# Kernel tuning notes

Measured on AMD Instinct MI355X. Metric: run time of the kernel, lower is better.

Reference implementation:

```python
import jax, jax.numpy as jnp
import numpy as np

BN_EPS = 1e-5
ALPHA = 0.3
NEG = -9e9
BN_SCALE = 1.0 / np.sqrt(1.0 + BN_EPS)  # eval BatchNorm with running_mean=0, running_var=1


def gat_layer(x, mask, W, a, bn_g, bn_b, concat):
    # x: [B,N,Fin], mask: [B,N,N] bool, W: [Fin,Fo], a: [2*Fo]
    h = jnp.einsum('bnf,fo->bno', x, W)               # [B,N,Fo]
    Fo = W.shape[1]
    s1 = h @ a[:Fo]                                    # [B,N]
    s2 = h @ a[Fo:]                                    # [B,N]
    # additive decomposition of concat([h_i, h_j]) @ a (identical math)
    e = jax.nn.leaky_relu(s1[:, :, None] + s2[:, None, :], ALPHA)  # [B,N,N]
    att = jax.nn.softmax(jnp.where(mask, e, NEG), axis=-1)
    hp = jnp.einsum('bnm,bmo->bno', att, h)            # [B,N,Fo]
    # BatchNorm1d(nodes_num) in eval mode, per-node-channel affine
    hp = hp * BN_SCALE * bn_g[None, :, None] + bn_b[None, :, None]
    return jax.nn.elu(hp) if concat else hp


def setup_inputs() -> dict:
    key = jax.random.key(0)
    ks = jax.random.split(key, 10)
    B, N, F, Fo, H, C = 128, 200, 768, 32, 8, 2
    Fh = Fo * H
    return {
        'feat_matrix': jax.random.normal(ks[0], (B, N, F), jnp.float32),
        'adj': jax.random.randint(ks[1], (B, N, N), 0, 2, jnp.int32),
        'W_heads': jax.random.normal(ks[2], (H, F, Fo), jnp.float32) * 0.05,
        'a_heads': jax.random.normal(ks[3], (H, 2 * Fo), jnp.float32) * 0.1,
        'bnh_g': jnp.ones((H, N), jnp.float32),
        'bnh_b': jnp.zeros((H, N), jnp.float32),
        'bnt_g': jnp.ones((N,), jnp.float32),
        'bnt_b': jnp.zeros((N,), jnp.float32),
        'W_sent': jax.random.normal(ks[4], (Fh, C), jnp.float32) * 0.1,
        'a_sent': jax.random.normal(ks[5], (2 * C,), jnp.float32) * 0.1,
        'bns_g': jnp.ones((N,), jnp.float32),
        'bns_b': jnp.zeros((N,), jnp.float32),
        'W_para': jax.random.normal(ks[6], (Fh, C), jnp.float32) * 0.1,
        'a_para': jax.random.normal(ks[7], (2 * C,), jnp.float32) * 0.1,
        'bnp_g': jnp.ones((N,), jnp.float32),
        'bnp_b': jnp.zeros((N,), jnp.float32),
        'W_q': jax.random.normal(ks[8], (Fh, Fo), jnp.float32) * 0.1,
        'a_q': jax.random.normal(ks[9], (2 * Fo,), jnp.float32) * 0.1,
        'bnq_g': jnp.ones((N,), jnp.float32),
        'bnq_b': jnp.zeros((N,), jnp.float32),
        'W2': jax.random.normal(jax.random.fold_in(key, 99), (Fo, 2), jnp.float32) * 0.1,
    }


def reference(feat_matrix, adj, W_heads, a_heads, bnh_g, bnh_b, bnt_g, bnt_b,
              W_sent, a_sent, bns_g, bns_b, W_para, a_para, bnp_g, bnp_b,
              W_q, a_q, bnq_g, bnq_b, W2):
    mask = adj > 0
    # 8 attention heads (concat=True), vmapped over head dim
    heads = jax.vmap(lambda W, a, g, b: gat_layer(feat_matrix, mask, W, a, g, b, True))(
        W_heads, a_heads, bnh_g, bnh_b)              # [H,B,N,Fo]
    H, B, N, Fo = heads.shape
    x = jnp.moveaxis(heads, 0, 2).reshape(B, N, H * Fo)  # head-major concat, matches torch.cat
    # top-level BatchNorm1d (eval) + dropout(no-op)
    x = x * BN_SCALE * bnt_g[None, :, None] + bnt_b[None, :, None]
    logits_sent = jax.nn.sigmoid(gat_layer(x, mask, W_sent, a_sent, bns_g, bns_b, False))
    logits_para = jax.nn.elu(gat_layer(x, mask, W_para, a_para, bnp_g, bnp_b, False))
    q = gat_layer(x, mask, W_q, a_q, bnq_g, bnq_b, False)[:, 0, :]   # [B,Fo]
    logits_Qtype = jax.nn.elu(q @ W2).reshape(-1, 2)
    return (logits_sent, logits_para, logits_Qtype)
```

## Files before the change

kernel.cpp:

```cpp
#include <hip/hip_runtime.h>
#include <hip/hip_bf16.h>
#include <cstdint>

#define BN_SCALEF 0.99999500003749975f
#define EXP_SHIFT 4.0f


typedef _Float16 half8 __attribute__((ext_vector_type(8)));
typedef _Float16 half4 __attribute__((ext_vector_type(4)));
typedef float floatx4 __attribute__((ext_vector_type(4)));


__global__ void pack_mask(const int* __restrict__ adj, unsigned int* __restrict__ maskw) {
    int bi = blockIdx.x;
    int t  = threadIdx.x;
    bool v = false;
    if (t < 200) v = adj[(size_t)bi * 200 + t] > 0;
    unsigned long long m = __ballot(v ? 1 : 0);
    if ((t & 63) == 0) {
        maskw[bi * 8 + (t >> 6) * 2 + 0] = (unsigned int)(m & 0xffffffffULL);
        maskw[bi * 8 + (t >> 6) * 2 + 1] = (unsigned int)(m >> 32);
    }
}

__global__ void build_wcat_t(const float* __restrict__ W_heads, _Float16* __restrict__ Bt) {
    int c = blockIdx.x;
    int h = c >> 5, o = c & 31;
    for (int f = threadIdx.x; f < 768; f += 256)
        Bt[(size_t)c * 768 + f] = (_Float16)W_heads[h * (768 * 32) + f * 32 + o];
}

__global__ void build_w2t(const float* __restrict__ Ws, const float* __restrict__ Wp,
                          const float* __restrict__ Wq, float* __restrict__ W2t) {
    int c = blockIdx.x;
    int k = threadIdx.x;
    float v;
    if (c < 2)      v = Ws[k * 2 + c];
    else if (c < 4) v = Wp[k * 2 + (c - 2)];
    else            v = Wq[k * 32 + (c - 4)];
    W2t[c * 256 + k] = v;
}


__global__ __launch_bounds__(512) void gemm1_mfma(const float* __restrict__ A,
                                                  const _Float16* __restrict__ Bt,
                                                  const float* __restrict__ a_h,
                                                  float* __restrict__ C,
                                                  float* __restrict__ s1,
                                                  float* __restrict__ s2) {
    __shared__ __align__(16) _Float16 As[128 * 40];
    __shared__ __align__(16) _Float16 Bs[256 * 40];
    int t = threadIdx.x;
    int m0 = blockIdx.x * 128;
    int w = t >> 6, lane = t & 63;
    int wr = w >> 2, wc = w & 3;
    int quad = lane >> 4, l16 = lane & 15;

    floatx4 acc[4][4];
#pragma unroll
    for (int i = 0; i < 4; ++i)
#pragma unroll
        for (int j = 0; j < 4; ++j) acc[i][j] = (floatx4){0.f, 0.f, 0.f, 0.f};

    int arow = t >> 2, akoff = (t & 3) * 8;
    int bcol = t >> 1, bkoff = (t & 1) * 16;
    const float*    Aptr = &A[(size_t)(m0 + arow) * 768 + akoff];
    const _Float16* Bptr = &Bt[(size_t)bcol * 768 + bkoff];

    float4 pa0 = *(const float4*)(Aptr);
    float4 pa1 = *(const float4*)(Aptr + 4);
    uint4  pb0 = *(const uint4*)(Bptr);
    uint4  pb1 = *(const uint4*)(Bptr + 8);

    for (int k0 = 0; k0 < 768; k0 += 32) {
        half8 ah;
        ah[0] = (_Float16)pa0.x; ah[1] = (_Float16)pa0.y;
        ah[2] = (_Float16)pa0.z; ah[3] = (_Float16)pa0.w;
        ah[4] = (_Float16)pa1.x; ah[5] = (_Float16)pa1.y;
        ah[6] = (_Float16)pa1.z; ah[7] = (_Float16)pa1.w;
        *(half8*)&As[arow * 40 + akoff] = ah;
        *(uint4*)&Bs[bcol * 40 + bkoff]     = pb0;
        *(uint4*)&Bs[bcol * 40 + bkoff + 8] = pb1;
        __syncthreads();
        if (k0 + 32 < 768) {
            pa0 = *(const float4*)(Aptr + k0 + 32);
            pa1 = *(const float4*)(Aptr + k0 + 36);
            pb0 = *(const uint4*)(Bptr + k0 + 32);
            pb1 = *(const uint4*)(Bptr + k0 + 40);
        }
        half8 af[4], bf[4];
#pragma unroll
        for (int rt = 0; rt < 4; ++rt)
            af[rt] = *(half8*)&As[(wr * 64 + rt * 16 + l16) * 40 + quad * 8];
#pragma unroll
        for (int ct = 0; ct < 4; ++ct)
            bf[ct] = *(half8*)&Bs[(wc * 64 + ct * 16 + l16) * 40 + quad * 8];
#pragma unroll
        for (int rt = 0; rt < 4; ++rt)
#pragma unroll
            for (int ct = 0; ct < 4; ++ct)
                acc[rt][ct] = __builtin_amdgcn_mfma_f32_16x16x32_f16(af[rt], bf[ct], acc[rt][ct], 0, 0, 0);
        __syncthreads();
    }

    int rbase = m0 + wr * 64;
    int cbase = wc * 64;
#pragma unroll
    for (int rt = 0; rt < 4; ++rt)
#pragma unroll
        for (int ct = 0; ct < 4; ++ct) {
            int gc = cbase + ct * 16 + l16;
#pragma unroll
            for (int r = 0; r < 4; ++r) {
                int gr = rbase + rt * 16 + quad * 4 + r;
                C[(size_t)gr * 256 + gc] = acc[rt][ct][r];
            }
        }
#pragma unroll
    for (int hh = 0; hh < 2; ++hh) {
        int h0 = wc * 2 + hh;
        const float* ab = &a_h[h0 * 64];
        float a1l = ab[l16], a1h = ab[16 + l16];
        float a2l = ab[32 + l16], a2h = ab[48 + l16];
#pragma unroll
        for (int rt = 0; rt < 4; ++rt)
#pragma unroll
            for (int r = 0; r < 4; ++r) {
                float v0 = acc[rt][2 * hh][r], v1 = acc[rt][2 * hh + 1][r];
                float p1 = v0 * a1l + v1 * a1h;
                float p2 = v0 * a2l + v1 * a2h;
                p1 += __shfl_xor(p1, 1, 64); p1 += __shfl_xor(p1, 2, 64);
                p1 += __shfl_xor(p1, 4, 64); p1 += __shfl_xor(p1, 8, 64);
                p2 += __shfl_xor(p2, 1, 64); p2 += __shfl_xor(p2, 2, 64);
                p2 += __shfl_xor(p2, 4, 64); p2 += __shfl_xor(p2, 8, 64);
                if (l16 == 0) {
                    int gr = rbase + rt * 16 + quad * 4 + r;
                    s1[h0 * 25600 + gr] = p1;
                    s2[h0 * 25600 + gr] = p2;
                }
            }
    }
}


__global__ __launch_bounds__(256) void attn_heads_mfma(
    const float* __restrict__ h_all, const float* __restrict__ s1g, const float* __restrict__ s2g,
    const unsigned int* __restrict__ maskw,
    const float* __restrict__ bnh_g, const float* __restrict__ bnh_b,
    const float* __restrict__ bnt_g, const float* __restrict__ bnt_b,
    float* __restrict__ x_cat) {
    __shared__ __align__(16) _Float16 Bs[48 * 232];
    __shared__ __align__(16) _Float16 Ps[64 * 232];
    int hb = blockIdx.x;
    int h = hb >> 7, b = hb & 127;
    int t = threadIdx.x;

    unsigned long long* bz = (unsigned long long*)Bs;
    for (int idx = t; idx < (48 * 232) / 4; idx += 256) bz[idx] = 0ULL;
    __syncthreads();
    for (int idx = t; idx < 1600; idx += 256) {
        int j = idx >> 3, w4 = (idx & 7) * 4;
        float4 v = *(const float4*)&h_all[(size_t)(b * 200 + j) * 256 + h * 32 + w4];
        Bs[(w4 + 0) * 232 + j] = (_Float16)v.x;
        Bs[(w4 + 1) * 232 + j] = (_Float16)v.y;
        Bs[(w4 + 2) * 232 + j] = (_Float16)v.z;
        Bs[(w4 + 3) * 232 + j] = (_Float16)v.w;
    }
    if (t < 200) Bs[32 * 232 + t] = (_Float16)1.0f;
    __syncthreads();

    int w = t >> 6, lane = t & 63;
    int l16 = lane & 15, quad = lane >> 4;
    _Float16* Pw = &Ps[w * 16 * 232];

    int j0 = lane * 4;
    float4 s2r = {0.f, 0.f, 0.f, 0.f};
    if (j0 + 3 < 200) {
        s2r = *(const float4*)&s2g[(size_t)(h * 128 + b) * 200 + j0];
    } else if (j0 < 200) {
        const float* sp = &s2g[(size_t)(h * 128 + b) * 200];
        float tmp[4] = {0.f, 0.f, 0.f, 0.f};
        for (int q = 0; q < 4 && j0 + q < 200; ++q) tmp[q] = sp[j0 + q];
        s2r = {tmp[0], tmp[1], tmp[2], tmp[3]};
    }
    const float* s1p = &s1g[(size_t)(h * 128 + b) * 200];

    for (int tile = w; tile < 13; tile += 4) {
        int i_base = tile * 16;
        int nrows = (i_base + 16 <= 200) ? 16 : (200 - i_base);
        for (int r16 = 0; r16 < nrows; ++r16) {
            int i = i_base + r16;
            float s1v = s1p[i];
            unsigned int mw = maskw[(size_t)(b * 200 + i) * 8 + (lane >> 3)];
            half4 pv;
#pragma unroll
            for (int q = 0; q < 4; ++q) {
                float e = s1v + ((const float*)&s2r)[q];
                e = fmaxf(e, 0.3f * e);
                float p = ((mw >> ((j0 + q) & 31)) & 1u) ? __expf(e - EXP_SHIFT) : 0.f;
                pv[q] = (_Float16)p;
            }
            if (j0 < 224) *(half4*)&Pw[r16 * 232 + j0] = pv;
        }
        floatx4 acc0 = {0.f, 0.f, 0.f, 0.f};
        floatx4 acc1 = {0.f, 0.f, 0.f, 0.f};
        floatx4 acc2 = {0.f, 0.f, 0.f, 0.f};
#pragma unroll
        for (int kt = 0; kt < 7; ++kt) {
            half8 af = *(half8*)&Pw[l16 * 232 + kt * 32 + quad * 8];
            half8 b0 = *(half8*)&Bs[(l16) * 232 + kt * 32 + quad * 8];
            half8 b1 = *(half8*)&Bs[(16 + l16) * 232 + kt * 32 + quad * 8];
            half8 b2 = *(half8*)&Bs[(32 + l16) * 232 + kt * 32 + quad * 8];
            acc0 = __builtin_amdgcn_mfma_f32_16x16x32_f16(af, b0, acc0, 0, 0, 0);
            acc1 = __builtin_amdgcn_mfma_f32_16x16x32_f16(af, b1, acc1, 0, 0, 0);
            acc2 = __builtin_amdgcn_mfma_f32_16x16x32_f16(af, b2, acc2, 0, 0, 0);
        }
#pragma unroll
        for (int r = 0; r < 4; ++r) {
            int i = i_base + quad * 4 + r;
            float rsum = __shfl(acc2[r], (lane & 48), 64);
            if (i < 200) {
                float inv = 1.f / rsum;
                float g1 = BN_SCALEF * bnh_g[h * 200 + i], c1 = bnh_b[h * 200 + i];
                float g2 = BN_SCALEF * bnt_g[i], c2 = bnt_b[i];
                float v0 = acc0[r] * inv * g1 + c1;
                v0 = v0 > 0.f ? v0 : __expf(v0) - 1.f;
                v0 = v0 * g2 + c2;
                float v1 = acc1[r] * inv * g1 + c1;
                v1 = v1 > 0.f ? v1 : __expf(v1) - 1.f;
                v1 = v1 * g2 + c2;
                size_t base = (size_t)(b * 200 + i) * 256 + h * 32;
                x_cat[base + l16]      = v0;
                x_cat[base + 16 + l16] = v1;
            }
        }
    }
}


__global__ __launch_bounds__(256) void gemm2(const float* __restrict__ X,
                                             const float* __restrict__ W2t,
                                             float* __restrict__ H2) {
    __shared__ __align__(16) float Ws[36 * 260];
    int t = threadIdx.x;
#pragma unroll
    for (int rep = 0; rep < 9; ++rep) {
        int fidx = rep * 1024 + t * 4;
        int c = fidx >> 8, k = fidx & 255;
        *(float4*)&Ws[c * 260 + k] = *(const float4*)&W2t[fidx];
    }
    __syncthreads();
    int cg = t & 3, rt = t >> 2;
    int row0 = blockIdx.x * 128 + rt * 2;
    float acc[2][9] = {};
#pragma unroll 2
    for (int k = 0; k < 256; k += 4) {
        float4 x0 = *(const float4*)&X[(size_t)row0 * 256 + k];
        float4 x1 = *(const float4*)&X[(size_t)(row0 + 1) * 256 + k];
#pragma unroll
        for (int c = 0; c < 9; ++c) {
            float4 wv = *(float4*)&Ws[(cg * 9 + c) * 260 + k];
            acc[0][c] += x0.x * wv.x + x0.y * wv.y + x0.z * wv.z + x0.w * wv.w;
            acc[1][c] += x1.x * wv.x + x1.y * wv.y + x1.z * wv.z + x1.w * wv.w;
        }
    }
#pragma unroll
    for (int rr = 0; rr < 2; ++rr)
#pragma unroll
        for (int c = 0; c < 9; ++c)
            H2[(size_t)(row0 + rr) * 36 + cg * 9 + c] = acc[rr][c];
}


__global__ __launch_bounds__(256) void s12_second(const float* __restrict__ H2,
                                                  const float* __restrict__ a_sent,
                                                  const float* __restrict__ a_para,
                                                  const float* __restrict__ a_q,
                                                  float* __restrict__ sv) {
    int row = blockIdx.x * 256 + threadIdx.x;
    const float* hp = &H2[(size_t)row * 36];
    float h0 = hp[0], h1 = hp[1], h2v = hp[2], h3 = hp[3];
    sv[row]          = h0 * a_sent[0] + h1 * a_sent[1];
    sv[25600 + row]  = h0 * a_sent[2] + h1 * a_sent[3];
    sv[51200 + row]  = h2v * a_para[0] + h3 * a_para[1];
    sv[76800 + row]  = h2v * a_para[2] + h3 * a_para[3];
    float aq1 = 0.f, aq2 = 0.f;
#pragma unroll
    for (int o = 0; o < 32; ++o) {
        float hv = hp[4 + o];
        aq1 += hv * a_q[o];
        aq2 += hv * a_q[32 + o];
    }
    sv[102400 + row] = aq1;
    sv[128000 + row] = aq2;
}


__global__ __launch_bounds__(256) void attn_sp(const float* __restrict__ H2,
                                               const float* __restrict__ sv,
                                               const unsigned int* __restrict__ maskw,
                                               const float* __restrict__ bns_g, const float* __restrict__ bns_b,
                                               const float* __restrict__ bnp_g, const float* __restrict__ bnp_b,
                                               float* __restrict__ out) {
    __shared__ float s2s[200], s2p[200];
    __shared__ __align__(16) float hsp[200 * 4];
    int b = blockIdx.x, chunk = blockIdx.y;
    int t = threadIdx.x;
    if (t < 200) {
        s2s[t] = sv[25600 + b * 200 + t];
        s2p[t] = sv[76800 + b * 200 + t];
    }
    for (int idx = t; idx < 800; idx += 256) {
        int j = idx >> 2, c = idx & 3;
        hsp[idx] = H2[(size_t)(b * 200 + j) * 36 + c];
    }
    __syncthreads();
    int w = t >> 6, lane = t & 63;
    for (int it = 0; it < 25; ++it) {
        int i = chunk * 100 + it * 4 + w;
        float s1sv = sv[b * 200 + i];
        float s1pv = sv[51200 + b * 200 + i];
        float ds = 0.f, dp = 0.f, pa0 = 0.f, pa1 = 0.f, pb0 = 0.f, pb1 = 0.f;
#pragma unroll
        for (int q = 0; q < 4; ++q) {
            int j = lane + 64 * q;
            if (j < 200) {
                unsigned int mw = maskw[(size_t)(b * 200 + i) * 8 + (j >> 5)];
                if ((mw >> (j & 31)) & 1u) {
                    float x1 = s1sv + s2s[j]; x1 = fmaxf(x1, 0.3f * x1);
                    float x2 = s1pv + s2p[j]; x2 = fmaxf(x2, 0.3f * x2);
                    float p1 = __expf(x1 - EXP_SHIFT), p2 = __expf(x2 - EXP_SHIFT);
                    ds += p1; dp += p2;
                    float4 hv = *(float4*)&hsp[j * 4];
                    pa0 += p1 * hv.x; pa1 += p1 * hv.y;
                    pb0 += p2 * hv.z; pb1 += p2 * hv.w;
                }
            }
        }
        for (int off = 32; off; off >>= 1) {
            ds  += __shfl_xor(ds, off, 64);  dp  += __shfl_xor(dp, off, 64);
            pa0 += __shfl_xor(pa0, off, 64); pa1 += __shfl_xor(pa1, off, 64);
            pb0 += __shfl_xor(pb0, off, 64); pb1 += __shfl_xor(pb1, off, 64);
        }
        if (lane == 0) {
            float gs = BN_SCALEF * bns_g[i], bs = bns_b[i];
            float v0 = (pa0 / ds) * gs + bs, v1 = (pa1 / ds) * gs + bs;
            out[(size_t)(b * 200 + i) * 2 + 0] = 1.f / (1.f + __expf(-v0));
            out[(size_t)(b * 200 + i) * 2 + 1] = 1.f / (1.f + __expf(-v1));
            float gp = BN_SCALEF * bnp_g[i], bp = bnp_b[i];
            float u0 = (pb0 / dp) * gp + bp, u1 = (pb1 / dp) * gp + bp;
            out[51200 + (size_t)(b * 200 + i) * 2 + 0] = u0 > 0.f ? u0 : __expf(u0) - 1.f;
            out[51200 + (size_t)(b * 200 + i) * 2 + 1] = u1 > 0.f ? u1 : __expf(u1) - 1.f;
        }
    }
}


__global__ __launch_bounds__(256) void attn_q(const float* __restrict__ H2,
                                              const float* __restrict__ sv,
                                              const unsigned int* __restrict__ maskw,
                                              const float* __restrict__ bnq_g, const float* __restrict__ bnq_b,
                                              const float* __restrict__ W2, float* __restrict__ out) {
    __shared__ float p_lds[200];
    __shared__ float redd[4];
    __shared__ float red2[256];
    int b = blockIdx.x, t = threadIdx.x;
    float s1v = sv[102400 + b * 200];
    float p = 0.f;
    if (t < 200) {
        unsigned int mw = maskw[(size_t)(b * 200) * 8 + (t >> 5)];
        if ((mw >> (t & 31)) & 1u) {
            float x = s1v + sv[128000 + b * 200 + t];
            x = fmaxf(x, 0.3f * x);
            p = __expf(x - EXP_SHIFT);
        }
        p_lds[t] = p;
    }
    float ds = p;
    for (int off = 32; off; off >>= 1) ds += __shfl_xor(ds, off, 64);
    if ((t & 63) == 0) redd[t >> 6] = ds;
    __syncthreads();
    ds = redd[0] + redd[1] + redd[2] + redd[3];
    int o = t & 31, g = t >> 5;
    float acc = 0.f;
    for (int j = g; j < 200; j += 8)
        acc += p_lds[j] * H2[(size_t)(b * 200 + j) * 36 + 4 + o];
    red2[t] = acc;
    __syncthreads();
    if (t < 32) {
        float s = 0.f;
#pragma unroll
        for (int gg = 0; gg < 8; ++gg) s += red2[gg * 32 + t];
        float qv = (s / ds) * (BN_SCALEF * bnq_g[0]) + bnq_b[0];
        float c0 = qv * W2[t * 2], c1 = qv * W2[t * 2 + 1];
#pragma unroll
        for (int off = 16; off; off >>= 1) {
            c0 += __shfl_xor(c0, off, 64);
            c1 += __shfl_xor(c1, off, 64);
        }
        if (t == 0) {
            out[102400 + b * 2 + 0] = c0 > 0.f ? c0 : __expf(c0) - 1.f;
            out[102400 + b * 2 + 1] = c1 > 0.f ? c1 : __expf(c1) - 1.f;
        }
    }
}


extern "C" void kernel_launch(void* const* d_in, const int* in_sizes, int n_in,
                              void* d_out, int out_size, void* d_ws, size_t ws_size,
                              hipStream_t stream) {
    (void)in_sizes; (void)n_in; (void)out_size; (void)ws_size;
    const float* feat    = (const float*)d_in[0];
    const int*   adj     = (const int*)d_in[1];
    const float* W_heads = (const float*)d_in[2];
    const float* a_heads = (const float*)d_in[3];
    const float* bnh_g   = (const float*)d_in[4];
    const float* bnh_b   = (const float*)d_in[5];
    const float* bnt_g   = (const float*)d_in[6];
    const float* bnt_b   = (const float*)d_in[7];
    const float* W_sent  = (const float*)d_in[8];
    const float* a_sent  = (const float*)d_in[9];
    const float* bns_g   = (const float*)d_in[10];
    const float* bns_b   = (const float*)d_in[11];
    const float* W_para  = (const float*)d_in[12];
    const float* a_para  = (const float*)d_in[13];
    const float* bnp_g   = (const float*)d_in[14];
    const float* bnp_b   = (const float*)d_in[15];
    const float* W_q     = (const float*)d_in[16];
    const float* a_q     = (const float*)d_in[17];
    const float* bnq_g   = (const float*)d_in[18];
    const float* bnq_b   = (const float*)d_in[19];
    const float* W2      = (const float*)d_in[20];
    float* out = (float*)d_out;
    float* ws  = (float*)d_ws;

    float* h_all = ws;
    float* x_cat = ws + 6553600;
    float* s1h   = ws + 13107200;
    float* s2h   = ws + 13312000;
    float* w2t   = ws + 13516800;
    _Float16* Bt = (_Float16*)(ws + 13526016);
    unsigned int* maskw = (unsigned int*)(ws + 13624320);
    float* h2    = ws + 13829120;
    float* sv    = ws + 14750720;

    pack_mask<<<dim3(25600), dim3(256), 0, stream>>>(adj, maskw);
    build_wcat_t<<<dim3(256), dim3(256), 0, stream>>>(W_heads, Bt);
    build_w2t<<<dim3(36), dim3(256), 0, stream>>>(W_sent, W_para, W_q, w2t);
    gemm1_mfma<<<dim3(200), dim3(512), 0, stream>>>(feat, Bt, a_heads, h_all, s1h, s2h);
    attn_heads_mfma<<<dim3(1024), dim3(256), 0, stream>>>(h_all, s1h, s2h, maskw,
                                                          bnh_g, bnh_b, bnt_g, bnt_b, x_cat);
    gemm2<<<dim3(200), dim3(256), 0, stream>>>(x_cat, w2t, h2);
    s12_second<<<dim3(100), dim3(256), 0, stream>>>(h2, a_sent, a_para, a_q, sv);
    attn_sp<<<dim3(128, 2), dim3(256), 0, stream>>>(h2, sv, maskw, bns_g, bns_b,
                                                    bnp_g, bnp_b, out);
    attn_q<<<dim3(128), dim3(256), 0, stream>>>(h2, sv, maskw, bnq_g, bnq_b, W2, out);
}
```

Before: 318.0 us.

## Merge prep kernels, store intermediates in fp16, shrink gemm1 tile, fuse tail kernels

Three preprocessing kernels become one prep kernel, and the W_heads transpose now goes through shared memory. gemm1 uses 64-row tiles, launching 400 blocks instead of 200 to fill more compute units. h and x_cat are stored as fp16 to halve the intermediate traffic. s12_second is fused into gemm2 and attn_q into attn_sp, cutting the launch count from 9 to 5. The risk is extra fp16 rounding in x_cat ahead of the second-layer GEMM.

Measured after the change: 299.9 us. 5.7% less time.

```diff
diff --git a/kernel.cpp b/kernel.cpp
--- a/kernel.cpp
+++ b/kernel.cpp
@@ -11,109 +11,123 @@
 typedef float floatx4 __attribute__((ext_vector_type(4)));
 
 
-__global__ void pack_mask(const int* __restrict__ adj, unsigned int* __restrict__ maskw) {
-    int bi = blockIdx.x;
-    int t  = threadIdx.x;
-    bool v = false;
-    if (t < 200) v = adj[(size_t)bi * 200 + t] > 0;
-    unsigned long long m = __ballot(v ? 1 : 0);
-    if ((t & 63) == 0) {
-        maskw[bi * 8 + (t >> 6) * 2 + 0] = (unsigned int)(m & 0xffffffffULL);
-        maskw[bi * 8 + (t >> 6) * 2 + 1] = (unsigned int)(m >> 32);
-    }
-}
-
-__global__ void build_wcat_t(const float* __restrict__ W_heads, _Float16* __restrict__ Bt) {
-    int c = blockIdx.x;
-    int h = c >> 5, o = c & 31;
-    for (int f = threadIdx.x; f < 768; f += 256)
-        Bt[(size_t)c * 768 + f] = (_Float16)W_heads[h * (768 * 32) + f * 32 + o];
-}
-
-__global__ void build_w2t(const float* __restrict__ Ws, const float* __restrict__ Wp,
-                          const float* __restrict__ Wq, float* __restrict__ W2t) {
-    int c = blockIdx.x;
-    int k = threadIdx.x;
-    float v;
-    if (c < 2)      v = Ws[k * 2 + c];
-    else if (c < 4) v = Wp[k * 2 + (c - 2)];
-    else            v = Wq[k * 32 + (c - 4)];
-    W2t[c * 256 + k] = v;
+__global__ __launch_bounds__(256) void prep(const int* __restrict__ adj,
+                                            const float* __restrict__ W_heads,
+                                            const float* __restrict__ Ws_in,
+                                            const float* __restrict__ Wp_in,
+                                            const float* __restrict__ Wq_in,
+                                            unsigned int* __restrict__ maskw,
+                                            _Float16* __restrict__ Bt,
+                                            float* __restrict__ W2t) {
+    int blk = blockIdx.x;
+    int t = threadIdx.x;
+    if (blk < 1600) {
+        int w = t >> 6, lane = t & 63;
+        for (int task = w; task < 64; task += 4) {
+            int r = blk * 16 + (task >> 2);
+            int c0 = (task & 3) * 64;
+            int j = c0 + lane;
+            bool v = (j < 200) && (adj[(size_t)r * 200 + j] > 0);
+            unsigned long long m = __ballot(v ? 1 : 0);
+            if (lane == 0) {
+                maskw[r * 8 + (c0 >> 5)]     = (unsigned int)(m & 0xffffffffULL);
+                maskw[r * 8 + (c0 >> 5) + 1] = (unsigned int)(m >> 32);
+            }
+        }
+    } else if (blk < 1792) {
+        __shared__ float ld[32][36];
+        int blk2 = blk - 1600;
+        int h = blk2 / 24, f0 = (blk2 % 24) * 32;
+        int idx = t * 4;
+        int fr = idx >> 5, o0 = idx & 31;
+        float4 v = *(const float4*)&W_heads[(size_t)h * 24576 + (size_t)(f0 + fr) * 32 + o0];
+        ld[fr][o0] = v.x; ld[fr][o0 + 1] = v.y; ld[fr][o0 + 2] = v.z; ld[fr][o0 + 3] = v.w;
+        __syncthreads();
+        int o = idx >> 5, fr0 = idx & 31;
+        half4 hv;
+#pragma unroll
+        for (int u = 0; u < 4; ++u) hv[u] = (_Float16)ld[fr0 + u][o];
+        *(half4*)&Bt[(size_t)(h * 32 + o) * 768 + f0 + fr0] = hv;
+    } else {
+        for (int c = 0; c < 36; ++c) {
+            float v;
+            if (c < 2)      v = Ws_in[t * 2 + c];
+            else if (c < 4) v = Wp_in[t * 2 + (c - 2)];
+            else            v = Wq_in[t * 32 + (c - 4)];
+            W2t[c * 256 + t] = v;
+        }
+    }
 }
 
 
 __global__ __launch_bounds__(512) void gemm1_mfma(const float* __restrict__ A,
                                                   const _Float16* __restrict__ Bt,
                                                   const float* __restrict__ a_h,
-                                                  float* __restrict__ C,
+                                                  _Float16* __restrict__ h16,
                                                   float* __restrict__ s1,
                                                   float* __restrict__ s2) {
-    __shared__ __align__(16) _Float16 As[128 * 40];
+    __shared__ __align__(16) _Float16 As[64 * 40];
     __shared__ __align__(16) _Float16 Bs[256 * 40];
     int t = threadIdx.x;
-    int m0 = blockIdx.x * 128;
+    int m0 = blockIdx.x * 64;
     int w = t >> 6, lane = t & 63;
     int wr = w >> 2, wc = w & 3;
     int quad = lane >> 4, l16 = lane & 15;
 
-    floatx4 acc[4][4];
-#pragma unroll
-    for (int i = 0; i < 4; ++i)
+    floatx4 acc[2][4];
+#pragma unroll
+    for (int i = 0; i < 2; ++i)
 #pragma unroll
         for (int j = 0; j < 4; ++j) acc[i][j] = (floatx4){0.f, 0.f, 0.f, 0.f};
 
-    int arow = t >> 2, akoff = (t & 3) * 8;
+    int arow = t >> 3, akoff = (t & 7) * 4;
     int bcol = t >> 1, bkoff = (t & 1) * 16;
     const float*    Aptr = &A[(size_t)(m0 + arow) * 768 + akoff];
     const _Float16* Bptr = &Bt[(size_t)bcol * 768 + bkoff];
 
-    float4 pa0 = *(const float4*)(Aptr);
-    float4 pa1 = *(const float4*)(Aptr + 4);
+    float4 pa  = *(const float4*)(Aptr);
     uint4  pb0 = *(const uint4*)(Bptr);
     uint4  pb1 = *(const uint4*)(Bptr + 8);
 
     for (int k0 = 0; k0 < 768; k0 += 32) {
-        half8 ah;
-        ah[0] = (_Float16)pa0.x; ah[1] = (_Float16)pa0.y;
-        ah[2] = (_Float16)pa0.z; ah[3] = (_Float16)pa0.w;
-        ah[4] = (_Float16)pa1.x; ah[5] = (_Float16)pa1.y;
-        ah[6] = (_Float16)pa1.z; ah[7] = (_Float16)pa1.w;
-        *(half8*)&As[arow * 40 + akoff] = ah;
+        half4 ah;
+        ah[0] = (_Float16)pa.x; ah[1] = (_Float16)pa.y;
+        ah[2] = (_Float16)pa.z; ah[3] = (_Float16)pa.w;
+        *(half4*)&As[arow * 40 + akoff] = ah;
         *(uint4*)&Bs[bcol * 40 + bkoff]     = pb0;
         *(uint4*)&Bs[bcol * 40 + bkoff + 8] = pb1;
         __syncthreads();
         if (k0 + 32 < 768) {
-            pa0 = *(const float4*)(Aptr + k0 + 32);
-            pa1 = *(const float4*)(Aptr + k0 + 36);
+            pa  = *(const float4*)(Aptr + k0 + 32);
             pb0 = *(const uint4*)(Bptr + k0 + 32);
             pb1 = *(const uint4*)(Bptr + k0 + 40);
         }
-        half8 af[4], bf[4];
-#pragma unroll
-        for (int rt = 0; rt < 4; ++rt)
-            af[rt] = *(half8*)&As[(wr * 64 + rt * 16 + l16) * 40 + quad * 8];
+        half8 af[2], bf[4];
+#pragma unroll
+        for (int rt = 0; rt < 2; ++rt)
+            af[rt] = *(half8*)&As[(wr * 32 + rt * 16 + l16) * 40 + quad * 8];
 #pragma unroll
         for (int ct = 0; ct < 4; ++ct)
             bf[ct] = *(half8*)&Bs[(wc * 64 + ct * 16 + l16) * 40 + quad * 8];
 #pragma unroll
-        for (int rt = 0; rt < 4; ++rt)
+        for (int rt = 0; rt < 2; ++rt)
 #pragma unroll
             for (int ct = 0; ct < 4; ++ct)
                 acc[rt][ct] = __builtin_amdgcn_mfma_f32_16x16x32_f16(af[rt], bf[ct], acc[rt][ct], 0, 0, 0);
         __syncthreads();
     }
 
-    int rbase = m0 + wr * 64;
+    int rbase = m0 + wr * 32;
     int cbase = wc * 64;
 #pragma unroll
-    for (int rt = 0; rt < 4; ++rt)
+    for (int rt = 0; rt < 2; ++rt)
 #pragma unroll
         for (int ct = 0; ct < 4; ++ct) {
             int gc = cbase + ct * 16 + l16;
 #pragma unroll
             for (int r = 0; r < 4; ++r) {
                 int gr = rbase + rt * 16 + quad * 4 + r;
-                C[(size_t)gr * 256 + gc] = acc[rt][ct][r];
+                h16[(size_t)gr * 256 + gc] = (_Float16)acc[rt][ct][r];
             }
         }
 #pragma unroll
@@ -123,7 +137,7 @@
         float a1l = ab[l16], a1h = ab[16 + l16];
         float a2l = ab[32 + l16], a2h = ab[48 + l16];
 #pragma unroll
-        for (int rt = 0; rt < 4; ++rt)
+        for (int rt = 0; rt < 2; ++rt)
 #pragma unroll
             for (int r = 0; r < 4; ++r) {
                 float v0 = acc[rt][2 * hh][r], v1 = acc[rt][2 * hh + 1][r];
@@ -144,11 +158,11 @@
 
 
 __global__ __launch_bounds__(256) void attn_heads_mfma(
-    const float* __restrict__ h_all, const float* __restrict__ s1g, const float* __restrict__ s2g,
+    const _Float16* __restrict__ h16, const float* __restrict__ s1g, const float* __restrict__ s2g,
     const unsigned int* __restrict__ maskw,
     const float* __restrict__ bnh_g, const float* __restrict__ bnh_b,
     const float* __restrict__ bnt_g, const float* __restrict__ bnt_b,
-    float* __restrict__ x_cat) {
+    _Float16* __restrict__ x16) {
     __shared__ __align__(16) _Float16 Bs[48 * 232];
     __shared__ __align__(16) _Float16 Ps[64 * 232];
     int hb = blockIdx.x;
@@ -158,13 +172,11 @@
     unsigned long long* bz = (unsigned long long*)Bs;
     for (int idx = t; idx < (48 * 232) / 4; idx += 256) bz[idx] = 0ULL;
     __syncthreads();
-    for (int idx = t; idx < 1600; idx += 256) {
-        int j = idx >> 3, w4 = (idx & 7) * 4;
-        float4 v = *(const float4*)&h_all[(size_t)(b * 200 + j) * 256 + h * 32 + w4];
-        Bs[(w4 + 0) * 232 + j] = (_Float16)v.x;
-        Bs[(w4 + 1) * 232 + j] = (_Float16)v.y;
-        Bs[(w4 + 2) * 232 + j] = (_Float16)v.z;
-        Bs[(w4 + 3) * 232 + j] = (_Float16)v.w;
+    for (int idx = t; idx < 800; idx += 256) {
+        int j = idx >> 2, w8 = (idx & 3) * 8;
+        half8 v = *(const half8*)&h16[(size_t)(b * 200 + j) * 256 + h * 32 + w8];
+#pragma unroll
+        for (int u = 0; u < 8; ++u) Bs[(w8 + u) * 232 + j] = v[u];
     }
     if (t < 200) Bs[32 * 232 + t] = (_Float16)1.0f;
     __syncthreads();
@@ -230,18 +242,23 @@
                 v1 = v1 > 0.f ? v1 : __expf(v1) - 1.f;
                 v1 = v1 * g2 + c2;
                 size_t base = (size_t)(b * 200 + i) * 256 + h * 32;
-                x_cat[base + l16]      = v0;
-                x_cat[base + 16 + l16] = v1;
-            }
-        }
-    }
-}
-
-
-__global__ __launch_bounds__(256) void gemm2(const float* __restrict__ X,
-                                             const float* __restrict__ W2t,
-                                             float* __restrict__ H2) {
+                x16[base + l16]      = (_Float16)v0;
+                x16[base + 16 + l16] = (_Float16)v1;
+            }
+        }
+    }
+}
+
+
+__global__ __launch_bounds__(256) void gemm2s(const _Float16* __restrict__ X,
+                                              const float* __restrict__ W2t,
+                                              const float* __restrict__ a_sent,
+                                              const float* __restrict__ a_para,
+                                              const float* __restrict__ a_q,
+                                              float* __restrict__ H2,
+                                              float* __restrict__ sv) {
     __shared__ __align__(16) float Ws[36 * 260];
+    __shared__ float Hs[128][37];
     int t = threadIdx.x;
 #pragma unroll
     for (int rep = 0; rep < 9; ++rep) {
@@ -253,59 +270,107 @@
     int cg = t & 3, rt = t >> 2;
     int row0 = blockIdx.x * 128 + rt * 2;
     float acc[2][9] = {};
-#pragma unroll 2
-    for (int k = 0; k < 256; k += 4) {
-        float4 x0 = *(const float4*)&X[(size_t)row0 * 256 + k];
-        float4 x1 = *(const float4*)&X[(size_t)(row0 + 1) * 256 + k];
+    for (int k = 0; k < 256; k += 8) {
+        half8 x0 = *(const half8*)&X[(size_t)row0 * 256 + k];
+        half8 x1 = *(const half8*)&X[(size_t)(row0 + 1) * 256 + k];
+        float xf0[8], xf1[8];
+#pragma unroll
+        for (int u = 0; u < 8; ++u) { xf0[u] = (float)x0[u]; xf1[u] = (float)x1[u]; }
 #pragma unroll
         for (int c = 0; c < 9; ++c) {
-            float4 wv = *(float4*)&Ws[(cg * 9 + c) * 260 + k];
-            acc[0][c] += x0.x * wv.x + x0.y * wv.y + x0.z * wv.z + x0.w * wv.w;
-            acc[1][c] += x1.x * wv.x + x1.y * wv.y + x1.z * wv.z + x1.w * wv.w;
+            const float* wr = &Ws[(cg * 9 + c) * 260 + k];
+            float4 wa = *(float4*)wr;
+            float4 wb = *(float4*)(wr + 4);
+            acc[0][c] += xf0[0] * wa.x + xf0[1] * wa.y + xf0[2] * wa.z + xf0[3] * wa.w
+                       + xf0[4] * wb.x + xf0[5] * wb.y + xf0[6] * wb.z + xf0[7] * wb.w;
+            acc[1][c] += xf1[0] * wa.x + xf1[1] * wa.y + xf1[2] * wa.z + xf1[3] * wa.w
+                       + xf1[4] * wb.x + xf1[5] * wb.y + xf1[6] * wb.z + xf1[7] * wb.w;
         }
     }
 #pragma unroll
     for (int rr = 0; rr < 2; ++rr)
 #pragma unroll
-        for (int c = 0; c < 9; ++c)
+        for (int c = 0; c < 9; ++c) {
             H2[(size_t)(row0 + rr) * 36 + cg * 9 + c] = acc[rr][c];
-}
-
-
-__global__ __launch_bounds__(256) void s12_second(const float* __restrict__ H2,
-                                                  const float* __restrict__ a_sent,
-                                                  const float* __restrict__ a_para,
-                                                  const float* __restrict__ a_q,
-                                                  float* __restrict__ sv) {
-    int row = blockIdx.x * 256 + threadIdx.x;
-    const float* hp = &H2[(size_t)row * 36];
-    float h0 = hp[0], h1 = hp[1], h2v = hp[2], h3 = hp[3];
-    sv[row]          = h0 * a_sent[0] + h1 * a_sent[1];
-    sv[25600 + row]  = h0 * a_sent[2] + h1 * a_sent[3];
-    sv[51200 + row]  = h2v * a_para[0] + h3 * a_para[1];
-    sv[76800 + row]  = h2v * a_para[2] + h3 * a_para[3];
-    float aq1 = 0.f, aq2 = 0.f;
-#pragma unroll
-    for (int o = 0; o < 32; ++o) {
-        float hv = hp[4 + o];
-        aq1 += hv * a_q[o];
-        aq2 += hv * a_q[32 + o];
-    }
-    sv[102400 + row] = aq1;
-    sv[128000 + row] = aq2;
-}
-
-
-__global__ __launch_bounds__(256) void attn_sp(const float* __restrict__ H2,
-                                               const float* __restrict__ sv,
-                                               const unsigned int* __restrict__ maskw,
-                                               const float* __restrict__ bns_g, const float* __restrict__ bns_b,
-                                               const float* __restrict__ bnp_g, const float* __restrict__ bnp_b,
-                                               float* __restrict__ out) {
+            Hs[rt * 2 + rr][cg * 9 + c] = acc[rr][c];
+        }
+    __syncthreads();
+    if (t < 128) {
+        int row = blockIdx.x * 128 + t;
+        float h0 = Hs[t][0], h1 = Hs[t][1], h2v = Hs[t][2], h3 = Hs[t][3];
+        sv[row]          = h0 * a_sent[0] + h1 * a_sent[1];
+        sv[25600 + row]  = h0 * a_sent[2] + h1 * a_sent[3];
+        sv[51200 + row]  = h2v * a_para[0] + h3 * a_para[1];
+        sv[76800 + row]  = h2v * a_para[2] + h3 * a_para[3];
+        float aq1 = 0.f, aq2 = 0.f;
+#pragma unroll
+        for (int o = 0; o < 32; ++o) {
+            float hv = Hs[t][4 + o];
+            aq1 += hv * a_q[o];
+            aq2 += hv * a_q[32 + o];
+        }
+        sv[102400 + row] = aq1;
+        sv[128000 + row] = aq2;
+    }
+}
+
+
+__global__ __launch_bounds__(256) void attn_spq(const float* __restrict__ H2,
+                                                const float* __restrict__ sv,
+                                                const unsigned int* __restrict__ maskw,
+                                                const float* __restrict__ bns_g, const float* __restrict__ bns_b,
+                                                const float* __restrict__ bnp_g, const float* __restrict__ bnp_b,
+                                                const float* __restrict__ bnq_g, const float* __restrict__ bnq_b,
+                                                const float* __restrict__ W2, float* __restrict__ out) {
+    int b = blockIdx.x;
+    int t = threadIdx.x;
+    if (blockIdx.y == 2) {
+        __shared__ float p_lds[200];
+        __shared__ float redd[4];
+        __shared__ float red2[256];
+        float s1v = sv[102400 + b * 200];
+        float p = 0.f;
+        if (t < 200) {
+            unsigned int mw = maskw[(size_t)(b * 200) * 8 + (t >> 5)];
+            if ((mw >> (t & 31)) & 1u) {
+                float x = s1v + sv[128000 + b * 200 + t];
+                x = fmaxf(x, 0.3f * x);
+                p = __expf(x - EXP_SHIFT);
+            }
+            p_lds[t] = p;
+        }
+        float ds = p;
+        for (int off = 32; off; off >>= 1) ds += __shfl_xor(ds, off, 64);
+        if ((t & 63) == 0) redd[t >> 6] = ds;
+        __syncthreads();
+        ds = redd[0] + redd[1] + redd[2] + redd[3];
+        int o = t & 31, g = t >> 5;
+        float acc = 0.f;
+        for (int j = g; j < 200; j += 8)
+            acc += p_lds[j] * H2[(size_t)(b * 200 + j) * 36 + 4 + o];
+        red2[t] = acc;
+        __syncthreads();
+        if (t < 32) {
+            float s = 0.f;
+#pragma unroll
+            for (int gg = 0; gg < 8; ++gg) s += red2[gg * 32 + t];
+            float qv = (s / ds) * (BN_SCALEF * bnq_g[0]) + bnq_b[0];
+            float c0 = qv * W2[t * 2], c1 = qv * W2[t * 2 + 1];
+#pragma unroll
+            for (int off = 16; off; off >>= 1) {
+                c0 += __shfl_xor(c0, off, 64);
+                c1 += __shfl_xor(c1, off, 64);
+            }
+            if (t == 0) {
+                out[102400 + b * 2 + 0] = c0 > 0.f ? c0 : __expf(c0) - 1.f;
+                out[102400 + b * 2 + 1] = c1 > 0.f ? c1 : __expf(c1) - 1.f;
+            }
+        }
+        return;
+    }
     __shared__ float s2s[200], s2p[200];
     __shared__ __align__(16) float hsp[200 * 4];
-    int b = blockIdx.x, chunk = blockIdx.y;
-    int t = threadIdx.x;
+    int chunk = blockIdx.y;
     if (t < 200) {
         s2s[t] = sv[25600 + b * 200 + t];
         s2p[t] = sv[76800 + b * 200 + t];
@@ -351,56 +416,6 @@
             float u0 = (pb0 / dp) * gp + bp, u1 = (pb1 / dp) * gp + bp;
             out[51200 + (size_t)(b * 200 + i) * 2 + 0] = u0 > 0.f ? u0 : __expf(u0) - 1.f;
             out[51200 + (size_t)(b * 200 + i) * 2 + 1] = u1 > 0.f ? u1 : __expf(u1) - 1.f;
-        }
-    }
-}
-
-
-__global__ __launch_bounds__(256) void attn_q(const float* __restrict__ H2,
-                                              const float* __restrict__ sv,
-                                              const unsigned int* __restrict__ maskw,
-                                              const float* __restrict__ bnq_g, const float* __restrict__ bnq_b,
-                                              const float* __restrict__ W2, float* __restrict__ out) {
-    __shared__ float p_lds[200];
-    __shared__ float redd[4];
-    __shared__ float red2[256];
-    int b = blockIdx.x, t = threadIdx.x;
-    float s1v = sv[102400 + b * 200];
-    float p = 0.f;
-    if (t < 200) {
-        unsigned int mw = maskw[(size_t)(b * 200) * 8 + (t >> 5)];
-        if ((mw >> (t & 31)) & 1u) {
-            float x = s1v + sv[128000 + b * 200 + t];
-            x = fmaxf(x, 0.3f * x);
-            p = __expf(x - EXP_SHIFT);
-        }
-        p_lds[t] = p;
-    }
-    float ds = p;
-    for (int off = 32; off; off >>= 1) ds += __shfl_xor(ds, off, 64);
-    if ((t & 63) == 0) redd[t >> 6] = ds;
-    __syncthreads();
-    ds = redd[0] + redd[1] + redd[2] + redd[3];
-    int o = t & 31, g = t >> 5;
-    float acc = 0.f;
-    for (int j = g; j < 200; j += 8)
-        acc += p_lds[j] * H2[(size_t)(b * 200 + j) * 36 + 4 + o];
-    red2[t] = acc;
-    __syncthreads();
-    if (t < 32) {
-        float s = 0.f;
-#pragma unroll
-        for (int gg = 0; gg < 8; ++gg) s += red2[gg * 32 + t];
-        float qv = (s / ds) * (BN_SCALEF * bnq_g[0]) + bnq_b[0];
-        float c0 = qv * W2[t * 2], c1 = qv * W2[t * 2 + 1];
-#pragma unroll
-        for (int off = 16; off; off >>= 1) {
-            c0 += __shfl_xor(c0, off, 64);
-            c1 += __shfl_xor(c1, off, 64);
-        }
-        if (t == 0) {
-            out[102400 + b * 2 + 0] = c0 > 0.f ? c0 : __expf(c0) - 1.f;
-            out[102400 + b * 2 + 1] = c1 > 0.f ? c1 : __expf(c1) - 1.f;
         }
     }
 }
@@ -434,25 +449,22 @@
     float* out = (float*)d_out;
     float* ws  = (float*)d_ws;
 
-    float* h_all = ws;
-    float* x_cat = ws + 6553600;
-    float* s1h   = ws + 13107200;
-    float* s2h   = ws + 13312000;
-    float* w2t   = ws + 13516800;
-    _Float16* Bt = (_Float16*)(ws + 13526016);
-    unsigned int* maskw = (unsigned int*)(ws + 13624320);
-    float* h2    = ws + 13829120;
-    float* sv    = ws + 14750720;
-
-    pack_mask<<<dim3(25600), dim3(256), 0, stream>>>(adj, maskw);
-    build_wcat_t<<<dim3(256), dim3(256), 0, stream>>>(W_heads, Bt);
-    build_w2t<<<dim3(36), dim3(256), 0, stream>>>(W_sent, W_para, W_q, w2t);
-    gemm1_mfma<<<dim3(200), dim3(512), 0, stream>>>(feat, Bt, a_heads, h_all, s1h, s2h);
-    attn_heads_mfma<<<dim3(1024), dim3(256), 0, stream>>>(h_all, s1h, s2h, maskw,
-                                                          bnh_g, bnh_b, bnt_g, bnt_b, x_cat);
-    gemm2<<<dim3(200), dim3(256), 0, stream>>>(x_cat, w2t, h2);
-    s12_second<<<dim3(100), dim3(256), 0, stream>>>(h2, a_sent, a_para, a_q, sv);
-    attn_sp<<<dim3(128, 2), dim3(256), 0, stream>>>(h2, sv, maskw, bns_g, bns_b,
-                                                    bnp_g, bnp_b, out);
-    attn_q<<<dim3(128), dim3(256), 0, stream>>>(h2, sv, maskw, bnq_g, bnq_b, W2, out);
-}
+    _Float16* h16 = (_Float16*)ws;
+    _Float16* x16 = (_Float16*)(ws + 3276800);
+    float* s1h   = ws + 6553600;
+    float* s2h   = ws + 6758400;
+    float* w2t   = ws + 6963200;
+    _Float16* Bt = (_Float16*)(ws + 6972416);
+    unsigned int* maskw = (unsigned int*)(ws + 7070720);
+    float* h2    = ws + 7275520;
+    float* sv    = ws + 8197120;
+
+    prep<<<dim3(1793), dim3(256), 0, stream>>>(adj, W_heads, W_sent, W_para, W_q,
+                                               maskw, Bt, w2t);
+    gemm1_mfma<<<dim3(400), dim3(512), 0, stream>>>(feat, Bt, a_heads, h16, s1h, s2h);
+    attn_heads_mfma<<<dim3(1024), dim3(256), 0, stream>>>(h16, s1h, s2h, maskw,
+                                                          bnh_g, bnh_b, bnt_g, bnt_b, x16);
+    gemm2s<<<dim3(200), dim3(256), 0, stream>>>(x16, w2t, a_sent, a_para, a_q, h2, sv);
+    attn_spq<<<dim3(128, 3), dim3(256), 0, stream>>>(h2, sv, maskw, bns_g, bns_b,
+                                                     bnp_g, bnp_b, bnq_g, bnq_b, W2, out);
+}
```
